# Performance work log

Measured on AMD Instinct MI355X. Metric: run time of the kernel, lower is better.

The kernel has to match this reference:

```python
import jax, jax.numpy as jnp
import numpy as np

M, K, O = 8192, 4096, 4096
WORDS = K // 32
INT32_MAX = 2147483647


def _unpack_ternary(nz, sgn):
    """Unpack bit-packed ternary weights.
    nz, sgn: [O, WORDS] int32 bitmasks. Bit j of word w corresponds to input
    column w*32 + j. weight = 0 if nz bit clear, else +1 (sgn bit clear) or -1.
    Returns dense float32 [O, K].
    """
    shifts = jnp.arange(32, dtype=jnp.uint32)
    nzb = (nz.astype(jnp.uint32)[:, :, None] >> shifts) & jnp.uint32(1)   # [O, WORDS, 32]
    sgb = (sgn.astype(jnp.uint32)[:, :, None] >> shifts) & jnp.uint32(1)  # [O, WORDS, 32]
    w = nzb.astype(jnp.float32) * (1.0 - 2.0 * sgb.astype(jnp.float32))
    return w.reshape(nz.shape[0], -1)  # [O, K]


def setup_inputs() -> dict:
    key = jax.random.key(0)
    k1, k2, k3, k4, k5 = jax.random.split(key, 5)
    x = jax.random.normal(k1, (M, K), dtype=jnp.float32)
    nz = jax.random.randint(k2, (O, WORDS), 0, INT32_MAX, dtype=jnp.int32)
    sgn = jax.random.randint(k3, (O, WORDS), 0, INT32_MAX, dtype=jnp.int32)
    bias = jax.random.normal(k4, (O,), dtype=jnp.float32) * 0.01
    alpha = jax.random.uniform(k5, (O,), dtype=jnp.float32, minval=0.5, maxval=1.5)
    return {"x": x, "nz": nz, "sgn": sgn, "bias": bias, "alpha": alpha}


def reference(x, nz, sgn, bias, alpha):
    # y = (x @ W^T) * alpha + bias, W dequantized from ternary bit-packs
    W = _unpack_ternary(nz, sgn)                       # [O, K]
    y = jnp.einsum('mk,ok->mo', x, W)                  # [M, O]
    y = y * alpha[None, :] + bias[None, :]
    return y
```

## Files before the change

kernel.cpp:

```cpp
#include <hip/hip_runtime.h>
#include <stdint.h>

#define M_DIM 8192
#define K_DIM 4096
#define O_DIM 4096
#define NWORDS 128

#define BM 128
#define BN 128
#define BK 64

typedef __attribute__((ext_vector_type(8))) short bf16x8;
typedef __attribute__((ext_vector_type(4))) float f32x4;
typedef __attribute__((ext_vector_type(4))) float fvec4;
typedef __attribute__((ext_vector_type(4))) unsigned uvec4;
typedef __attribute__((ext_vector_type(2))) unsigned uvec2;

__device__ __forceinline__ unsigned f32_to_bf16u(float f) {
  union { float f; unsigned u; } v; v.f = f;
  return (v.u + 0x7FFFu + ((v.u >> 16) & 1u)) >> 16;
}

__device__ __forceinline__ unsigned pack_bf16x2(float lo, float hi) {
  return f32_to_bf16u(lo) | (f32_to_bf16u(hi) << 16);
}

__global__ __launch_bounds__(256) void prep_kernel(const fvec4* __restrict__ x,
                                                   uvec2* __restrict__ xb,
                                                   const unsigned* __restrict__ nz,
                                                   const unsigned* __restrict__ sgn,
                                                   unsigned short* __restrict__ wb) {
  const int b   = blockIdx.x;
  const int tid = threadIdx.x;
  if (b < 8192) {
    const long base = (long)b * 1024 + tid;
#pragma unroll
    for (int j = 0; j < 4; ++j) {
      const long g = base + j * 256;
      const fvec4 v = x[g];
      uvec2 o;
      o.x = pack_bf16x2(v.x, v.y);
      o.y = pack_bf16x2(v.z, v.w);
      xb[g] = o;
    }
  } else {
    const int i = (b - 8192) * 256 + tid;
    const int w = i >> 2;
    const int q = i & 3;
    const unsigned n = nz[w] >> (8 * q);
    const unsigned s = sgn[w] >> (8 * q);
    unsigned out[4];
#pragma unroll
    for (int p = 0; p < 4; ++p) {
      const int j0 = 2 * p, j1 = 2 * p + 1;
      unsigned lo = ((n >> j0) & 1u) ? (0x3F80u | (((s >> j0) & 1u) << 15)) : 0u;
      unsigned hi = ((n >> j1) & 1u) ? (0x3F80u | (((s >> j1) & 1u) << 15)) : 0u;
      out[p] = lo | (hi << 16);
    }
    uvec4 v = { out[0], out[1], out[2], out[3] };
    *(uvec4*)(wb + (long)w * 32 + q * 8) = v;
  }
}

__global__ __launch_bounds__(256) void gemm_kernel(const unsigned short* __restrict__ A,
                                                   const unsigned short* __restrict__ B,
                                                   const float* __restrict__ bias,
                                                   const float* __restrict__ alpha,
                                                   float* __restrict__ C) {
  __shared__ unsigned short lA[BM * BK];
  __shared__ unsigned short lB[BN * BK];

  const int tid  = threadIdx.x;
  const int lane = tid & 63;
  const int wave = tid >> 6;
  const int mBlk = blockIdx.y * BM;
  const int nBlk = blockIdx.x * BN;

  int oArr[4];
  const unsigned short *gA[4], *gB[4];
#pragma unroll
  for (int j = 0; j < 4; ++j) {
    const int oj = tid * 16 + j * 4096;
    const int r  = oj >> 7;
    const int qp = (oj >> 4) & 7;
    const int q  = qp ^ (r & 7);
    gA[j] = A + (long)(mBlk + r) * K_DIM + q * 8;
    gB[j] = B + (long)(nBlk + r) * K_DIM + q * 8;
    oArr[j] = oj;
  }
  char* lAc = (char*)lA;
  char* lBc = (char*)lB;

  const int wm = (wave >> 1) * 64;
  const int wn = (wave & 1) * 64;
  const int fr = lane & 15;
  const int fq = lane >> 4;

  f32x4 acc[4][4] = {};

  for (int kt = 0; kt < K_DIM; kt += BK) {
#pragma unroll
    for (int j = 0; j < 4; ++j) {
      __builtin_amdgcn_global_load_lds((const __attribute__((address_space(1))) void*)(gA[j] + kt),
                                       (__attribute__((address_space(3))) void*)(lAc + oArr[j]), 16, 0, 0);
      __builtin_amdgcn_global_load_lds((const __attribute__((address_space(1))) void*)(gB[j] + kt),
                                       (__attribute__((address_space(3))) void*)(lBc + oArr[j]), 16, 0, 0);
    }
    __syncthreads();

#pragma unroll
    for (int kh = 0; kh < 2; ++kh) {
      bf16x8 af[4], bfv[4];
#pragma unroll
      for (int t = 0; t < 4; ++t) {
        const int rA = wm + t * 16 + fr;
        const int qA = (kh * 4 + fq) ^ (rA & 7);
        af[t] = *(const bf16x8*)(lA + rA * BK + qA * 8);
        const int rB = wn + t * 16 + fr;
        const int qB = (kh * 4 + fq) ^ (rB & 7);
        bfv[t] = *(const bf16x8*)(lB + rB * BK + qB * 8);
      }
#pragma unroll
      for (int tm = 0; tm < 4; ++tm)
#pragma unroll
        for (int tn = 0; tn < 4; ++tn)
          acc[tm][tn] = __builtin_amdgcn_mfma_f32_16x16x32_bf16(af[tm], bfv[tn], acc[tm][tn], 0, 0, 0);
    }
    __syncthreads();
  }

#pragma unroll
  for (int tn = 0; tn < 4; ++tn) {
    const int n = nBlk + wn + tn * 16 + fr;
    const float al = alpha[n];
    const float bi = bias[n];
#pragma unroll
    for (int tm = 0; tm < 4; ++tm) {
      const int mBase = mBlk + wm + tm * 16 + fq * 4;
#pragma unroll
      for (int r = 0; r < 4; ++r)
        __builtin_nontemporal_store(acc[tm][tn][r] * al + bi,
                                    C + (long)(mBase + r) * O_DIM + n);
    }
  }
}

__global__ __launch_bounds__(256) void fallback_kernel(const float* __restrict__ x,
                                                       const unsigned* __restrict__ nz,
                                                       const unsigned* __restrict__ sgn,
                                                       const float* __restrict__ bias,
                                                       const float* __restrict__ alpha,
                                                       float* __restrict__ y) {
  long gid = (long)blockIdx.x * 256 + threadIdx.x;
  int o = (int)(gid % O_DIM);
  long m = gid / O_DIM;
  const float* xr = x + m * K_DIM;
  float s = 0.f;
  for (int w = 0; w < NWORDS; ++w) {
    unsigned n = nz[o * NWORDS + w];
    unsigned g = sgn[o * NWORDS + w];
    for (int j = 0; j < 32; ++j) {
      if ((n >> j) & 1u) {
        float v = xr[w * 32 + j];
        s += ((g >> j) & 1u) ? -v : v;
      }
    }
  }
  y[gid] = s * alpha[o] + bias[o];
}

extern "C" void kernel_launch(void* const* d_in, const int* in_sizes, int n_in,
                              void* d_out, int out_size, void* d_ws, size_t ws_size,
                              hipStream_t stream) {
  const float*    x     = (const float*)d_in[0];
  const unsigned* nz    = (const unsigned*)d_in[1];
  const unsigned* sgn   = (const unsigned*)d_in[2];
  const float*    bias  = (const float*)d_in[3];
  const float*    alpha = (const float*)d_in[4];
  float*          y     = (float*)d_out;

  const size_t xb_bytes = (size_t)M_DIM * K_DIM * 2;
  const size_t wb_bytes = (size_t)O_DIM * K_DIM * 2;

  if (ws_size >= xb_bytes + wb_bytes) {
    unsigned short* xb = (unsigned short*)d_ws;
    unsigned short* wb = (unsigned short*)((char*)d_ws + xb_bytes);

    prep_kernel<<<16384, 256, 0, stream>>>((const fvec4*)x, (uvec2*)xb, nz, sgn, wb);
    dim3 grid(O_DIM / BN, M_DIM / BM);
    gemm_kernel<<<grid, 256, 0, stream>>>(xb, wb, bias, alpha, y);
  } else {
    fallback_kernel<<<(long)M_DIM * O_DIM / 256, 256, 0, stream>>>(x, nz, sgn, bias, alpha, y);
  }
}
```

Measured before the change: 488.6 us.

## Rewrite GEMM as 256x256 tile, 8-wave kernel with double-buffered LDS pipeline

Measured after the change: 436.9 us. 10.6% less time.

```diff
diff --git a/kernel.cpp b/kernel.cpp
--- a/kernel.cpp
+++ b/kernel.cpp
@@ -5,10 +5,6 @@
 #define K_DIM 4096
 #define O_DIM 4096
 #define NWORDS 128
-
-#define BM 128
-#define BN 128
-#define BK 64
 
 typedef __attribute__((ext_vector_type(8))) short bf16x8;
 typedef __attribute__((ext_vector_type(4))) float f32x4;
@@ -62,87 +58,152 @@
   }
 }
 
-__global__ __launch_bounds__(256) void gemm_kernel(const unsigned short* __restrict__ A,
-                                                   const unsigned short* __restrict__ B,
-                                                   const float* __restrict__ bias,
-                                                   const float* __restrict__ alpha,
-                                                   float* __restrict__ C) {
-  __shared__ unsigned short lA[BM * BK];
-  __shared__ unsigned short lB[BN * BK];
+__global__ __launch_bounds__(512, 2) void gemm_kernel(const unsigned short* __restrict__ A,
+                                                      const unsigned short* __restrict__ B,
+                                                      const float* __restrict__ bias,
+                                                      const float* __restrict__ alpha,
+                                                      float* __restrict__ C) {
+  __shared__ unsigned short lds[65536];
 
   const int tid  = threadIdx.x;
   const int lane = tid & 63;
   const int wave = tid >> 6;
-  const int mBlk = blockIdx.y * BM;
-  const int nBlk = blockIdx.x * BN;
-
-  int oArr[4];
-  const unsigned short *gA[4], *gB[4];
-#pragma unroll
-  for (int j = 0; j < 4; ++j) {
-    const int oj = tid * 16 + j * 4096;
-    const int r  = oj >> 7;
-    const int qp = (oj >> 4) & 7;
-    const int q  = qp ^ (r & 7);
-    gA[j] = A + (long)(mBlk + r) * K_DIM + q * 8;
-    gB[j] = B + (long)(nBlk + r) * K_DIM + q * 8;
-    oArr[j] = oj;
-  }
-  char* lAc = (char*)lA;
-  char* lBc = (char*)lB;
-
-  const int wm = (wave >> 1) * 64;
-  const int wn = (wave & 1) * 64;
-  const int fr = lane & 15;
-  const int fq = lane >> 4;
-
-  f32x4 acc[4][4] = {};
-
-  for (int kt = 0; kt < K_DIM; kt += BK) {
-#pragma unroll
-    for (int j = 0; j < 4; ++j) {
-      __builtin_amdgcn_global_load_lds((const __attribute__((address_space(1))) void*)(gA[j] + kt),
-                                       (__attribute__((address_space(3))) void*)(lAc + oArr[j]), 16, 0, 0);
-      __builtin_amdgcn_global_load_lds((const __attribute__((address_space(1))) void*)(gB[j] + kt),
-                                       (__attribute__((address_space(3))) void*)(lBc + oArr[j]), 16, 0, 0);
-    }
-    __syncthreads();
-
-#pragma unroll
-    for (int kh = 0; kh < 2; ++kh) {
-      bf16x8 af[4], bfv[4];
-#pragma unroll
-      for (int t = 0; t < 4; ++t) {
-        const int rA = wm + t * 16 + fr;
-        const int qA = (kh * 4 + fq) ^ (rA & 7);
-        af[t] = *(const bf16x8*)(lA + rA * BK + qA * 8);
-        const int rB = wn + t * 16 + fr;
-        const int qB = (kh * 4 + fq) ^ (rB & 7);
-        bfv[t] = *(const bf16x8*)(lB + rB * BK + qB * 8);
-      }
-#pragma unroll
-      for (int tm = 0; tm < 4; ++tm)
-#pragma unroll
-        for (int tn = 0; tn < 4; ++tn)
-          acc[tm][tn] = __builtin_amdgcn_mfma_f32_16x16x32_bf16(af[tm], bfv[tn], acc[tm][tn], 0, 0, 0);
-    }
-    __syncthreads();
-  }
+  const int wm   = wave >> 2;
+  const int wn   = wave & 3;
+
+  const int wg   = blockIdx.x;
+  const int swz  = (wg & 7) * 64 + (wg >> 3);
+  const int nBlk = (swz & 15) * 256;
+  const int mBlk = (swz >> 4) * 256;
+
+  const unsigned short* Apan = A + (long)mBlk * K_DIM;
+  const unsigned short* Bpan = B + (long)nBlk * K_DIM;
+
+  int lOff[2], gOff[2];
+#pragma unroll
+  for (int l = 0; l < 2; ++l) {
+    const int o = (l * 512 + tid) * 16;
+    const int r = o >> 7;
+    const int q = ((o >> 4) & 7) ^ (r & 7);
+    lOff[l] = o;
+    gOff[l] = r * K_DIM + q * 8;
+  }
+
+  const int fr  = lane & 15;
+  const int fq  = lane >> 4;
+  const int sl0 = fq ^ (fr & 7);
+  const int aFB = fr * 64;
+  const int bFB = (wn & 1) * 4096 + fr * 64;
+  const int A0S = wm * 8192;
+  const int A1S = (2 + wm) * 8192;
+  const int B0S = 32768 + (wn >> 1) * 8192;
+  const int B1S = 32768 + (2 + (wn >> 1)) * 8192;
+
+  f32x4  acc[8][4] = {};
+  bf16x8 a[4][2], bv[4][2];
+
+#define STAGE(SUBv, BUFv, TILEv) do {                                          \
+    const unsigned short* s_ = (((SUBv) < 2) ? Apan : Bpan)                    \
+        + (long)((SUBv) & 1) * (128 * K_DIM) + (long)(TILEv) * 64;             \
+    const int dB = ((((SUBv) < 2) ? 0 : 32768)                                 \
+        + (((BUFv) * 2) + ((SUBv) & 1)) * 8192) * 2;                           \
+    __builtin_amdgcn_global_load_lds(                                          \
+        (const __attribute__((address_space(1))) void*)(s_ + gOff[0]),         \
+        (__attribute__((address_space(3))) void*)((char*)lds + dB + lOff[0]),  \
+        16, 0, 0);                                                             \
+    __builtin_amdgcn_global_load_lds(                                          \
+        (const __attribute__((address_space(1))) void*)(s_ + gOff[1]),         \
+        (__attribute__((address_space(3))) void*)((char*)lds + dB + lOff[1]),  \
+        16, 0, 0);                                                             \
+  } while (0)
+
+#define LOADA(BASE, TQ)                                                        \
+  _Pragma("unroll")                                                            \
+  for (int i = 0; i < 4; ++i) {                                                \
+    const int off_ = (BASE) + ((TQ) * 4 + i) * 1024 + aFB;                     \
+    a[i][0] = *(const bf16x8*)(lds + off_ + sl0 * 8);                          \
+    a[i][1] = *(const bf16x8*)(lds + off_ + (sl0 ^ 4) * 8);                    \
+  }
+
+#define LOADB(BASE)                                                            \
+  _Pragma("unroll")                                                            \
+  for (int j = 0; j < 4; ++j) {                                                \
+    const int off_ = (BASE) + bFB + j * 1024;                                  \
+    bv[j][0] = *(const bf16x8*)(lds + off_ + sl0 * 8);                         \
+    bv[j][1] = *(const bf16x8*)(lds + off_ + (sl0 ^ 4) * 8);                   \
+  }
+
+#define MFMAQ(QM, QN)                                                          \
+  _Pragma("unroll")                                                            \
+  for (int kh = 0; kh < 2; ++kh)                                               \
+    _Pragma("unroll")                                                          \
+    for (int i = 0; i < 4; ++i)                                                \
+      _Pragma("unroll")                                                        \
+      for (int j = 0; j < 2; ++j)                                              \
+        acc[(QM) * 4 + i][(QN) * 2 + j] = __builtin_amdgcn_mfma_f32_16x16x32_bf16( \
+            a[i][kh], bv[(QN) * 2 + j][kh], acc[(QM) * 4 + i][(QN) * 2 + j], 0, 0, 0);
+
+#define MID()  __builtin_amdgcn_s_barrier();                                   \
+               asm volatile("s_waitcnt lgkmcnt(0)" ::: "memory");              \
+               __builtin_amdgcn_s_setprio(1)
+#define ENDPH()   __builtin_amdgcn_s_setprio(0); __builtin_amdgcn_s_barrier()
+#define ENDVM6()  __builtin_amdgcn_s_setprio(0);                               \
+                  asm volatile("s_waitcnt vmcnt(6)" ::: "memory");             \
+                  __builtin_amdgcn_s_barrier()
+#define ENDVM0()  __builtin_amdgcn_s_setprio(0);                               \
+                  asm volatile("s_waitcnt vmcnt(0)" ::: "memory");             \
+                  __builtin_amdgcn_s_barrier()
+
+  STAGE(2, 0, 0); STAGE(3, 0, 0); STAGE(0, 0, 0); STAGE(1, 0, 0);
+  STAGE(2, 1, 1); STAGE(3, 1, 1); STAGE(0, 1, 1);
+  asm volatile("s_waitcnt vmcnt(6)" ::: "memory");
+  __builtin_amdgcn_s_barrier();
+
+  for (int it = 0; it < (K_DIM / 64) / 2 - 1; ++it) {
+    const int t1 = 2 * it + 1, t2 = 2 * it + 2, t3 = 2 * it + 3;
+    LOADA(A0S, 0); LOADB(B0S); STAGE(1, 1, t1); MID(); MFMAQ(0, 0); ENDPH();
+                               STAGE(2, 0, t2); MID(); MFMAQ(0, 1); ENDPH();
+    LOADA(A0S, 1);             STAGE(3, 0, t2); MID(); MFMAQ(1, 0); ENDPH();
+                               STAGE(0, 0, t2); MID(); MFMAQ(1, 1); ENDVM6();
+    LOADA(A1S, 0); LOADB(B1S); STAGE(1, 0, t2); MID(); MFMAQ(0, 0); ENDPH();
+                               STAGE(2, 1, t3); MID(); MFMAQ(0, 1); ENDPH();
+    LOADA(A1S, 1);             STAGE(3, 1, t3); MID(); MFMAQ(1, 0); ENDPH();
+                               STAGE(0, 1, t3); MID(); MFMAQ(1, 1); ENDVM6();
+  }
+
+  LOADA(A0S, 0); LOADB(B0S); STAGE(1, 1, 63); MID(); MFMAQ(0, 0); ENDPH();
+                                              MID(); MFMAQ(0, 1); ENDPH();
+  LOADA(A0S, 1);                              MID(); MFMAQ(1, 0); ENDPH();
+                                              MID(); MFMAQ(1, 1); ENDVM0();
+  LOADA(A1S, 0); LOADB(B1S);                  MID(); MFMAQ(0, 0); ENDPH();
+                                              MID(); MFMAQ(0, 1); ENDPH();
+  LOADA(A1S, 1);                              MID(); MFMAQ(1, 0); ENDPH();
+                                              MID(); MFMAQ(1, 1);
+  __builtin_amdgcn_s_setprio(0);
 
 #pragma unroll
   for (int tn = 0; tn < 4; ++tn) {
-    const int n = nBlk + wn + tn * 16 + fr;
+    const int n = nBlk + wn * 64 + tn * 16 + fr;
     const float al = alpha[n];
     const float bi = bias[n];
 #pragma unroll
-    for (int tm = 0; tm < 4; ++tm) {
-      const int mBase = mBlk + wm + tm * 16 + fq * 4;
+    for (int tm = 0; tm < 8; ++tm) {
+      const int mBase = mBlk + wm * 128 + tm * 16 + fq * 4;
 #pragma unroll
       for (int r = 0; r < 4; ++r)
         __builtin_nontemporal_store(acc[tm][tn][r] * al + bi,
                                     C + (long)(mBase + r) * O_DIM + n);
     }
   }
+
+#undef STAGE
+#undef LOADA
+#undef LOADB
+#undef MFMAQ
+#undef MID
+#undef ENDPH
+#undef ENDVM6
+#undef ENDVM0
 }
 
 __global__ __launch_bounds__(256) void fallback_kernel(const float* __restrict__ x,
@@ -187,8 +248,7 @@
     unsigned short* wb = (unsigned short*)((char*)d_ws + xb_bytes);
 
     prep_kernel<<<16384, 256, 0, stream>>>((const fvec4*)x, (uvec2*)xb, nz, sgn, wb);
-    dim3 grid(O_DIM / BN, M_DIM / BM);
-    gemm_kernel<<<grid, 256, 0, stream>>>(xb, wb, bias, alpha, y);
+    gemm_kernel<<<512, 512, 0, stream>>>(xb, wb, bias, alpha, y);
   } else {
     fallback_kernel<<<(long)M_DIM * O_DIM / 256, 256, 0, stream>>>(x, nz, sgn, bias, alpha, y);
   }
```
